# Performance work log

Measured on AMD Instinct MI355X. Metric: run time of the kernel, lower is better.

The kernel has to match this reference:

```python
import jax, jax.numpy as jnp
import numpy as np

B, T, E, H, L = 256, 150, 512, 8, 6
Dh = E // H
FF = 4 * E
NC = 4  # num_decision_classes


def _layer_norm(x, g, b, eps=1e-5):
    m = jnp.mean(x, -1, keepdims=True)
    v = jnp.mean((x - m) ** 2, -1, keepdims=True)
    return (x - m) * jax.lax.rsqrt(v + eps) * g + b


def setup_inputs():
    key = jax.random.key(0)
    ks = jax.random.split(key, 24)
    std = 0.02
    return {
        'token_type': jax.random.randint(ks[0], (B, T), 0, 3, dtype=jnp.int32),
        'mask': jax.random.randint(ks[1], (B, T), 0, 2, dtype=jnp.int32),
        'decision_idx': jax.random.randint(ks[2], (B, T), 0, NC, dtype=jnp.int32),
        'action_val': jax.random.normal(ks[3], (B, T, 1), jnp.float32),
        'dis_val': jax.random.normal(ks[4], (B, T, 10), jnp.float32),
        'v_val': jax.random.normal(ks[5], (B, T, 3), jnp.float32),
        'action_W': jax.random.normal(ks[6], (1, E), jnp.float32) * std,
        'action_b': jnp.zeros((E,), jnp.float32),
        'dis_W': jax.random.normal(ks[7], (10, E), jnp.float32) * std,
        'dis_b': jnp.zeros((E,), jnp.float32),
        'v_W': jax.random.normal(ks[8], (3, E), jnp.float32) * std,
        'v_b': jnp.zeros((E,), jnp.float32),
        'dec_emb': jax.random.normal(ks[9], (NC, E), jnp.float32) * std,
        'pos_embed': jax.random.normal(ks[10], (1, T + 1, E), jnp.float32) * std,
        'cls_token': jax.random.normal(ks[11], (1, 1, E), jnp.float32) * std,
        'qkv_W': jax.random.normal(ks[12], (L, E, 3 * E), jnp.float32) * std,
        'qkv_b': jnp.zeros((L, 3 * E), jnp.float32),
        'out_W': jax.random.normal(ks[13], (L, E, E), jnp.float32) * std,
        'out_b': jnp.zeros((L, E), jnp.float32),
        'ln1_g': jnp.ones((L, E), jnp.float32),
        'ln1_b': jnp.zeros((L, E), jnp.float32),
        'ff1_W': jax.random.normal(ks[14], (L, E, FF), jnp.float32) * std,
        'ff1_b': jnp.zeros((L, FF), jnp.float32),
        'ff2_W': jax.random.normal(ks[15], (L, FF, E), jnp.float32) * std,
        'ff2_b': jnp.zeros((L, E), jnp.float32),
        'ln2_g': jnp.ones((L, E), jnp.float32),
        'ln2_b': jnp.zeros((L, E), jnp.float32),
    }


def reference(token_type, mask, decision_idx, action_val, dis_val, v_val,
              action_W, action_b, dis_W, dis_b, v_W, v_b, dec_emb,
              pos_embed, cls_token, qkv_W, qkv_b, out_W, out_b,
              ln1_g, ln1_b, ff1_W, ff1_b, ff2_W, ff2_b, ln2_g, ln2_b):
    Bx, Tx = token_type.shape
    # vectorized per-type token embedding dispatch (A / S / D)
    a = action_val @ action_W + action_b                       # [B,T,E]
    s = dis_val @ dis_W + dis_b + v_val @ v_W + v_b            # [B,T,E]
    d = dec_emb[decision_idx]                                  # [B,T,E]
    tt = token_type[..., None]
    x = jnp.where(tt == 0, a, jnp.where(tt == 1, s, d))
    x = x + pos_embed[:, :Tx, :]
    x = jnp.concatenate([jnp.broadcast_to(cls_token, (Bx, 1, x.shape[-1])), x], axis=1)
    S = Tx + 1
    pad = jnp.concatenate([jnp.zeros((Bx, 1), bool), mask == 0], axis=1)  # True = padded key
    bias = jnp.where(pad, jnp.float32(-1e9), jnp.float32(0.0))[:, None, None, :]  # [B,1,1,S]
    scale = jnp.float32(1.0 / np.sqrt(Dh))

    def block(x, p):
        qkvW, qkvb, oW, ob, g1, b1, f1W, f1b, f2W, f2b, g2, b2 = p
        qkv = x @ qkvW + qkvb                                  # [B,S,3E]
        q, k, v = jnp.split(qkv, 3, axis=-1)
        hd = lambda t: t.reshape(Bx, S, H, Dh).transpose(0, 2, 1, 3)
        q, k, v = hd(q), hd(k), hd(v)                          # [B,H,S,Dh]
        scores = jnp.einsum('bhqd,bhkd->bhqk', q, k) * scale + bias
        attn = jax.nn.softmax(scores, axis=-1)
        o = jnp.einsum('bhqk,bhkd->bhqd', attn, v).transpose(0, 2, 1, 3).reshape(Bx, S, -1)
        x = _layer_norm(x + o @ oW + ob, g1, b1)               # post-norm (torch default)
        h = jax.nn.relu(x @ f1W + f1b) @ f2W + f2b
        x = _layer_norm(x + h, g2, b2)
        return x, None

    params = (qkv_W, qkv_b, out_W, out_b, ln1_g, ln1_b,
              ff1_W, ff1_b, ff2_W, ff2_b, ln2_g, ln2_b)
    x, _ = jax.lax.scan(block, x, params)
    return x[:, 0, :]  # cls output, mode='pretrain'
```

## Files before the change

### kernel.cpp

```cpp
#include <hip/hip_runtime.h>
#include <hip/hip_bf16.h>
#include <stdint.h>

#define B_ 256
#define T_ 150
#define S_ 151
#define E_ 512
#define H_ 8
#define L_ 6
#define FF_ 2048
#define M_ (B_*S_)

typedef __hip_bfloat16 bf16;
typedef __bf16 bf16x8 __attribute__((ext_vector_type(8)));
typedef float f32x4 __attribute__((ext_vector_type(4)));
typedef unsigned short u16x8 __attribute__((ext_vector_type(8)));

__device__ inline unsigned short f2b(float x) {
    union { __hip_bfloat16 h; unsigned short u; } c;
    c.h = __float2bfloat16(x);
    return c.u;
}
__device__ inline float b2f(unsigned short u) {
    union { uint32_t u; float f; } c;
    c.u = (uint32_t)u << 16;
    return c.f;
}

__device__ __forceinline__ void gl16(const void* g, void* l) {
    __builtin_amdgcn_global_load_lds(
        (const __attribute__((address_space(1))) unsigned int*)g,
        (__attribute__((address_space(3))) unsigned int*)l, 16, 0, 0);
}

__global__ __launch_bounds__(256)
void transpose_cast_kernel(const float* __restrict__ src, bf16* __restrict__ dst,
                           int K, int N) {
    __shared__ float tile[64][65];
    int l = blockIdx.z;
    const float* s = src + (size_t)l * K * N;
    bf16* d = dst + (size_t)l * K * N;
    int bk = blockIdx.x * 64, bn = blockIdx.y * 64;
    int col = threadIdx.x & 63, rg = threadIdx.x >> 6;
#pragma unroll
    for (int i = 0; i < 16; ++i) {
        int r = i * 4 + rg;
        tile[r][col] = s[(size_t)(bk + r) * N + bn + col];
    }
    __syncthreads();
#pragma unroll
    for (int i = 0; i < 16; ++i) {
        int r = i * 4 + rg;
        d[(size_t)(bn + r) * K + bk + col] = __float2bfloat16(tile[col][r]);
    }
}

__global__ __launch_bounds__(256)
void embed_kernel(const int* __restrict__ tt, const int* __restrict__ dec_idx,
                  const float* __restrict__ action_val, const float* __restrict__ dis_val,
                  const float* __restrict__ v_val,
                  const float* __restrict__ action_W, const float* __restrict__ action_b,
                  const float* __restrict__ dis_W, const float* __restrict__ dis_b,
                  const float* __restrict__ v_W, const float* __restrict__ v_b,
                  const float* __restrict__ dec_emb, const float* __restrict__ pos,
                  const float* __restrict__ cls,
                  bf16* __restrict__ xbf) {
    int lane = threadIdx.x & 63;
    int bs = blockIdx.x * 4 + (threadIdx.x >> 6);
    int b = bs / S_, s = bs - b * S_;
    int e0 = lane * 8;
    f32x4 v0, v1;
    if (s == 0) {
        v0 = *(const f32x4*)(cls + e0);
        v1 = *(const f32x4*)(cls + e0 + 4);
    } else {
        int t = s - 1;
        int ty = tt[b * T_ + t];
        if (ty == 0) {
            float av = action_val[b * T_ + t];
            f32x4 w0 = *(const f32x4*)(action_W + e0);
            f32x4 w1 = *(const f32x4*)(action_W + e0 + 4);
            f32x4 b0 = *(const f32x4*)(action_b + e0);
            f32x4 b1 = *(const f32x4*)(action_b + e0 + 4);
            v0 = w0 * av + b0;  v1 = w1 * av + b1;
        } else if (ty == 1) {
            v0 = *(const f32x4*)(dis_b + e0) + *(const f32x4*)(v_b + e0);
            v1 = *(const f32x4*)(dis_b + e0 + 4) + *(const f32x4*)(v_b + e0 + 4);
#pragma unroll
            for (int i = 0; i < 10; ++i) {
                float dv = dis_val[(b * T_ + t) * 10 + i];
                v0 += *(const f32x4*)(dis_W + i * E_ + e0) * dv;
                v1 += *(const f32x4*)(dis_W + i * E_ + e0 + 4) * dv;
            }
#pragma unroll
            for (int i = 0; i < 3; ++i) {
                float vv = v_val[(b * T_ + t) * 3 + i];
                v0 += *(const f32x4*)(v_W + i * E_ + e0) * vv;
                v1 += *(const f32x4*)(v_W + i * E_ + e0 + 4) * vv;
            }
        } else {
            const float* de = dec_emb + (size_t)dec_idx[b * T_ + t] * E_;
            v0 = *(const f32x4*)(de + e0);
            v1 = *(const f32x4*)(de + e0 + 4);
        }
        v0 += *(const f32x4*)(pos + (size_t)t * E_ + e0);
        v1 += *(const f32x4*)(pos + (size_t)t * E_ + e0 + 4);
    }
    size_t o = (size_t)bs * E_ + e0;
    union { unsigned short s[8]; uint4 v; } pk;
    pk.s[0] = f2b(v0[0]); pk.s[1] = f2b(v0[1]); pk.s[2] = f2b(v0[2]); pk.s[3] = f2b(v0[3]);
    pk.s[4] = f2b(v1[0]); pk.s[5] = f2b(v1[1]); pk.s[6] = f2b(v1[2]); pk.s[7] = f2b(v1[3]);
    *(uint4*)((unsigned short*)xbf + o) = pk.v;
}

template<int MODE>
__global__ __launch_bounds__(256, 2)
void gemm_kernel(const bf16* __restrict__ A, const bf16* __restrict__ Bt,
                 const float* __restrict__ bias, bf16* __restrict__ Cb,
                 int N, int K) {
    __shared__ alignas(16) bf16 As[128][64];
    __shared__ alignas(16) bf16 Bs[128][64];
    const int tid = threadIdx.x;
    const int wave = tid >> 6, lane = tid & 63;
    const int nwg = gridDim.x, bid = blockIdx.x;
    const int Nt = N >> 7;
    const int q = nwg >> 3, r = nwg & 7;
    const int xcd = bid & 7, slot = bid >> 3;
    const int wgid = (xcd < r ? xcd * (q + 1) : r * (q + 1) + (xcd - r) * q) + slot;
    const int mt = wgid / Nt, ntl = wgid - mt * Nt;
    const int m0 = mt * 128, n0 = ntl * 128;
    const int wm = (wave >> 1) * 64, wn = (wave & 1) * 64;
    const int l15 = lane & 15, lg = lane >> 4;

    f32x4 acc[4][4] = {};

    for (int k0 = 0; k0 < K; k0 += 64) {
#pragma unroll
        for (int i = 0; i < 4; ++i) {
            int chunk = i * 256 + tid;
            int row = chunk >> 3, cl = chunk & 7;
            int gc = cl ^ (row & 7);
            gl16(A + (size_t)(m0 + row) * K + k0 + gc * 8,
                 (char*)&As[0][0] + chunk * 16);
            gl16(Bt + (size_t)(n0 + row) * K + k0 + gc * 8,
                 (char*)&Bs[0][0] + chunk * 16);
        }
        __syncthreads();
#pragma unroll
        for (int kf = 0; kf < 2; ++kf) {
            bf16x8 af[4], bfr[4];
#pragma unroll
            for (int mf = 0; mf < 4; ++mf) {
                int row = wm + mf * 16 + l15;
                int csw = (kf * 4 + lg) ^ (row & 7);
                af[mf] = *(const bf16x8*)((const char*)&As[0][0] + row * 128 + csw * 16);
            }
#pragma unroll
            for (int nf = 0; nf < 4; ++nf) {
                int row = wn + nf * 16 + l15;
                int csw = (kf * 4 + lg) ^ (row & 7);
                bfr[nf] = *(const bf16x8*)((const char*)&Bs[0][0] + row * 128 + csw * 16);
            }
#pragma unroll
            for (int mf = 0; mf < 4; ++mf)
#pragma unroll
                for (int nf = 0; nf < 4; ++nf)
                    acc[mf][nf] = __builtin_amdgcn_mfma_f32_16x16x32_bf16(
                        af[mf], bfr[nf], acc[mf][nf], 0, 0, 0);
        }
        __syncthreads();
    }
#pragma unroll
    for (int nf = 0; nf < 4; ++nf) {
        int col = n0 + wn + nf * 16 + l15;
        float bv = bias[col];
#pragma unroll
        for (int mf = 0; mf < 4; ++mf) {
#pragma unroll
            for (int j = 0; j < 4; ++j) {
                int row = m0 + wm + mf * 16 + lg * 4 + j;
                size_t idx = (size_t)row * N + col;
                float x = acc[mf][nf][j] + bv;
                if (MODE == 1) x = fmaxf(x, 0.f);
                Cb[idx] = __float2bfloat16(x);
            }
        }
    }
}

#define VP_ 168
__global__ __launch_bounds__(256, 2)
void attn_kernel(const bf16* __restrict__ qkv, const int* __restrict__ mask,
                 bf16* __restrict__ obf) {
    __shared__ alignas(16) unsigned short ldsbuf[32064];
    unsigned short* Kb = ldsbuf;
    unsigned short* QP = ldsbuf + 10240;
    unsigned short* Vt = ldsbuf + 10240 + 10752;
    float* biasf = (float*)(ldsbuf + 10240 + 10752 + 10752);

    const int bh = blockIdx.x;
    const int b = bh >> 3, h = bh & 7;
    const int tid = threadIdx.x, w = tid >> 6, lane = tid & 63;
    const int l15 = lane & 15, lg = lane >> 4;
    const size_t base = (size_t)b * S_ * 1536 + h * 64;
    const unsigned short* qk16 = (const unsigned short*)qkv;

    for (int i = tid; i < 160 * 8; i += 256) {
        int r = i >> 3, c = i & 7;
        int csw = c ^ (r & 7);
        uint4 kz = make_uint4(0u, 0u, 0u, 0u), qz = kz;
        if (r < 151) {
            kz = *(const uint4*)(qk16 + base + (size_t)r * 1536 + 512 + c * 8);
            qz = *(const uint4*)(qk16 + base + (size_t)r * 1536 + c * 8);
        }
        *(uint4*)((char*)Kb + r * 128 + csw * 16) = kz;
        *(uint4*)((char*)QP + r * 128 + csw * 16) = qz;
    }
    for (int i = tid; i < 160 * 8; i += 256) {
        int n = i >> 3, c = i & 7;
        u16x8 vv = {0, 0, 0, 0, 0, 0, 0, 0};
        if (n < 151) vv = *(const u16x8*)(qk16 + base + (size_t)n * 1536 + 1024 + c * 8);
#pragma unroll
        for (int e = 0; e < 8; ++e) Vt[(c * 8 + e) * VP_ + n] = vv[e];
    }
    if (tid < 160) {
        float bv;
        if (tid == 0) bv = 0.f;
        else if (tid <= 150) bv = (mask[b * T_ + tid - 1] != 0) ? 0.f : -1e9f;
        else bv = -1e9f;
        biasf[tid] = bv;
    }
    __syncthreads();

    int r0 = w * 16 + l15;
    int r1 = r0 + 64;
    int r2 = r0 + 128; if (r2 > 159) r2 = 159;
    bf16x8 q00 = *(const bf16x8*)((const char*)QP + r0 * 128 + ((lg)     ^ (r0 & 7)) * 16);
    bf16x8 q01 = *(const bf16x8*)((const char*)QP + r0 * 128 + ((4 + lg) ^ (r0 & 7)) * 16);
    bf16x8 q10 = *(const bf16x8*)((const char*)QP + r1 * 128 + ((lg)     ^ (r1 & 7)) * 16);
    bf16x8 q11 = *(const bf16x8*)((const char*)QP + r1 * 128 + ((4 + lg) ^ (r1 & 7)) * 16);
    bf16x8 q20 = *(const bf16x8*)((const char*)QP + r2 * 128 + ((lg)     ^ (r2 & 7)) * 16);
    bf16x8 q21 = *(const bf16x8*)((const char*)QP + r2 * 128 + ((4 + lg) ^ (r2 & 7)) * 16);
    float bc0 = biasf[l15],       bc1 = biasf[16 + l15],  bc2 = biasf[32 + l15];
    float bc3 = biasf[48 + l15],  bc4 = biasf[64 + l15],  bc5 = biasf[80 + l15];
    float bc6 = biasf[96 + l15],  bc7 = biasf[112 + l15], bc8 = biasf[128 + l15];
    float bc9 = biasf[144 + l15];
    __syncthreads();

    bf16* Pw = (bf16*)(QP + w * 16 * VP_);
    const float scale = 0.125f;

#pragma unroll
    for (int mi = 0; mi < 3; ++mi) {
        int mt = w + mi * 4;
        if (mt < 10) {
            bf16x8 qk0 = (mi == 0) ? q00 : (mi == 1) ? q10 : q20;
            bf16x8 qk1 = (mi == 0) ? q01 : (mi == 1) ? q11 : q21;
            f32x4 sc[10] = {};
#pragma unroll
            for (int nt = 0; nt < 10; ++nt) {
                int kr = nt * 16 + l15;
                bf16x8 kb0 = *(const bf16x8*)((const char*)Kb + kr * 128 + ((lg)     ^ (kr & 7)) * 16);
                bf16x8 kb1 = *(const bf16x8*)((const char*)Kb + kr * 128 + ((4 + lg) ^ (kr & 7)) * 16);
                sc[nt] = __builtin_amdgcn_mfma_f32_16x16x32_bf16(qk0, kb0, sc[nt], 0, 0, 0);
                sc[nt] = __builtin_amdgcn_mfma_f32_16x16x32_bf16(qk1, kb1, sc[nt], 0, 0, 0);
            }
            float m0r = -3e38f, m1r = -3e38f, m2r = -3e38f, m3r = -3e38f;
#pragma unroll
            for (int nt = 0; nt < 10; ++nt) {
                float bv = (nt == 0) ? bc0 : (nt == 1) ? bc1 : (nt == 2) ? bc2 :
                           (nt == 3) ? bc3 : (nt == 4) ? bc4 : (nt == 5) ? bc5 :
                           (nt == 6) ? bc6 : (nt == 7) ? bc7 : (nt == 8) ? bc8 : bc9;
                sc[nt][0] = sc[nt][0] * scale + bv;  m0r = fmaxf(m0r, sc[nt][0]);
                sc[nt][1] = sc[nt][1] * scale + bv;  m1r = fmaxf(m1r, sc[nt][1]);
                sc[nt][2] = sc[nt][2] * scale + bv;  m2r = fmaxf(m2r, sc[nt][2]);
                sc[nt][3] = sc[nt][3] * scale + bv;  m3r = fmaxf(m3r, sc[nt][3]);
            }
#pragma unroll
            for (int off = 1; off < 16; off <<= 1) {
                m0r = fmaxf(m0r, __shfl_xor(m0r, off));
                m1r = fmaxf(m1r, __shfl_xor(m1r, off));
                m2r = fmaxf(m2r, __shfl_xor(m2r, off));
                m3r = fmaxf(m3r, __shfl_xor(m3r, off));
            }
            float s0 = 0.f, s1 = 0.f, s2 = 0.f, s3 = 0.f;
#pragma unroll
            for (int nt = 0; nt < 10; ++nt) {
                sc[nt][0] = __expf(sc[nt][0] - m0r);  s0 += sc[nt][0];
                sc[nt][1] = __expf(sc[nt][1] - m1r);  s1 += sc[nt][1];
                sc[nt][2] = __expf(sc[nt][2] - m2r);  s2 += sc[nt][2];
                sc[nt][3] = __expf(sc[nt][3] - m3r);  s3 += sc[nt][3];
            }
#pragma unroll
            for (int off = 1; off < 16; off <<= 1) {
                s0 += __shfl_xor(s0, off);
                s1 += __shfl_xor(s1, off);
                s2 += __shfl_xor(s2, off);
                s3 += __shfl_xor(s3, off);
            }
            s0 = 1.f / s0; s1 = 1.f / s1; s2 = 1.f / s2; s3 = 1.f / s3;
#pragma unroll
            for (int nt = 0; nt < 10; ++nt) {
                int cb = nt * 16 + l15;
                Pw[(lg * 4 + 0) * VP_ + cb] = __float2bfloat16(sc[nt][0]);
                Pw[(lg * 4 + 1) * VP_ + cb] = __float2bfloat16(sc[nt][1]);
                Pw[(lg * 4 + 2) * VP_ + cb] = __float2bfloat16(sc[nt][2]);
                Pw[(lg * 4 + 3) * VP_ + cb] = __float2bfloat16(sc[nt][3]);
            }
            f32x4 oc[4] = {};
#pragma unroll
            for (int nc = 0; nc < 5; ++nc) {
                bf16x8 pa = *(const bf16x8*)((const unsigned short*)Pw + l15 * VP_ + nc * 32 + lg * 8);
#pragma unroll
                for (int dt = 0; dt < 4; ++dt) {
                    bf16x8 vb = *(const bf16x8*)(Vt + (dt * 16 + l15) * VP_ + nc * 32 + lg * 8);
                    oc[dt] = __builtin_amdgcn_mfma_f32_16x16x32_bf16(pa, vb, oc[dt], 0, 0, 0);
                }
            }
            int orow = mt * 16 + lg * 4;
#pragma unroll
            for (int dt = 0; dt < 4; ++dt) {
                int d = h * 64 + dt * 16 + l15;
                if (orow + 0 < 151) obf[((size_t)(b * S_ + orow + 0)) * E_ + d] = __float2bfloat16(oc[dt][0] * s0);
                if (orow + 1 < 151) obf[((size_t)(b * S_ + orow + 1)) * E_ + d] = __float2bfloat16(oc[dt][1] * s1);
                if (orow + 2 < 151) obf[((size_t)(b * S_ + orow + 2)) * E_ + d] = __float2bfloat16(oc[dt][2] * s2);
                if (orow + 3 < 151) obf[((size_t)(b * S_ + orow + 3)) * E_ + d] = __float2bfloat16(oc[dt][3] * s3);
            }
        }
    }
}

__global__ __launch_bounds__(256)
void ln_res_kernel(const bf16* __restrict__ t_bf, const float* __restrict__ gw,
                   const float* __restrict__ bw, bf16* __restrict__ xbf) {
    int lane = threadIdx.x & 63;
    int row = blockIdx.x * 4 + (threadIdx.x >> 6);
    size_t o = (size_t)row * E_ + lane * 8;
    u16x8 xv = *(const u16x8*)((const unsigned short*)xbf + o);
    u16x8 tv = *(const u16x8*)((const unsigned short*)t_bf + o);
    f32x4 t0, t1;
    t0[0] = b2f(xv[0]) + b2f(tv[0]); t0[1] = b2f(xv[1]) + b2f(tv[1]);
    t0[2] = b2f(xv[2]) + b2f(tv[2]); t0[3] = b2f(xv[3]) + b2f(tv[3]);
    t1[0] = b2f(xv[4]) + b2f(tv[4]); t1[1] = b2f(xv[5]) + b2f(tv[5]);
    t1[2] = b2f(xv[6]) + b2f(tv[6]); t1[3] = b2f(xv[7]) + b2f(tv[7]);
    float s = t0[0] + t0[1] + t0[2] + t0[3] + t1[0] + t1[1] + t1[2] + t1[3];
#pragma unroll
    for (int off = 1; off < 64; off <<= 1) s += __shfl_xor(s, off);
    float mean = s * (1.0f / 512.0f);
    f32x4 d0 = t0 - mean, d1 = t1 - mean;
    float q = d0[0]*d0[0] + d0[1]*d0[1] + d0[2]*d0[2] + d0[3]*d0[3]
            + d1[0]*d1[0] + d1[1]*d1[1] + d1[2]*d1[2] + d1[3]*d1[3];
#pragma unroll
    for (int off = 1; off < 64; off <<= 1) q += __shfl_xor(q, off);
    float rstd = rsqrtf(q * (1.0f / 512.0f) + 1e-5f);
    f32x4 g0 = *(const f32x4*)(gw + lane * 8);
    f32x4 g1 = *(const f32x4*)(gw + lane * 8 + 4);
    f32x4 bb0 = *(const f32x4*)(bw + lane * 8);
    f32x4 bb1 = *(const f32x4*)(bw + lane * 8 + 4);
    f32x4 y0 = d0 * rstd * g0 + bb0;
    f32x4 y1 = d1 * rstd * g1 + bb1;
    union { unsigned short s[8]; uint4 v; } pk;
    pk.s[0] = f2b(y0[0]); pk.s[1] = f2b(y0[1]); pk.s[2] = f2b(y0[2]); pk.s[3] = f2b(y0[3]);
    pk.s[4] = f2b(y1[0]); pk.s[5] = f2b(y1[1]); pk.s[6] = f2b(y1[2]); pk.s[7] = f2b(y1[3]);
    *(uint4*)((unsigned short*)xbf + o) = pk.v;
}

__global__ __launch_bounds__(256)
void out_kernel(const bf16* __restrict__ xbf, float* __restrict__ out) {
    int i = blockIdx.x * 256 + threadIdx.x;
    int b = i >> 9, e = i & 511;
    out[i] = b2f(((const unsigned short*)xbf)[(size_t)b * S_ * E_ + e]);
}

extern "C" void kernel_launch(void* const* d_in, const int* in_sizes, int n_in,
                              void* d_out, int out_size, void* d_ws, size_t ws_size,
                              hipStream_t stream) {
    (void)in_sizes; (void)n_in; (void)out_size; (void)ws_size;
    const int*   token_type = (const int*)d_in[0];
    const int*   mask       = (const int*)d_in[1];
    const int*   dec_idx    = (const int*)d_in[2];
    const float* action_val = (const float*)d_in[3];
    const float* dis_val    = (const float*)d_in[4];
    const float* v_val      = (const float*)d_in[5];
    const float* action_W   = (const float*)d_in[6];
    const float* action_b   = (const float*)d_in[7];
    const float* dis_W      = (const float*)d_in[8];
    const float* dis_b      = (const float*)d_in[9];
    const float* v_W        = (const float*)d_in[10];
    const float* v_b        = (const float*)d_in[11];
    const float* dec_emb    = (const float*)d_in[12];
    const float* pos        = (const float*)d_in[13];
    const float* cls        = (const float*)d_in[14];
    const float* qkv_W      = (const float*)d_in[15];
    const float* qkv_b      = (const float*)d_in[16];
    const float* out_W      = (const float*)d_in[17];
    const float* out_b      = (const float*)d_in[18];
    const float* ln1_g      = (const float*)d_in[19];
    const float* ln1_b      = (const float*)d_in[20];
    const float* ff1_W      = (const float*)d_in[21];
    const float* ff1_b      = (const float*)d_in[22];
    const float* ff2_W      = (const float*)d_in[23];
    const float* ff2_b      = (const float*)d_in[24];
    const float* ln2_g      = (const float*)d_in[25];
    const float* ln2_b      = (const float*)d_in[26];

    char* ws = (char*)d_ws;
    size_t off = 0;
    auto alloc = [&](size_t bytes) {
        char* p = ws + off;
        off += (bytes + 255) & ~(size_t)255;
        return p;
    };
    bf16* qkvT = (bf16*)alloc((size_t)L_ * 1536 * 512 * 2);
    bf16* outT = (bf16*)alloc((size_t)L_ * 512 * 512 * 2);
    bf16* ff1T = (bf16*)alloc((size_t)L_ * 2048 * 512 * 2);
    bf16* ff2T = (bf16*)alloc((size_t)L_ * 512 * 2048 * 2);
    bf16*  xbf = (bf16*)alloc((size_t)M_ * E_ * 2);
    bf16* arena = (bf16*)alloc((size_t)M_ * 2048 * 2);
    bf16* qkvbf  = arena;
    bf16* obf    = arena + (size_t)M_ * 1536;
    bf16* projout= arena;
    bf16* hbf    = arena + (size_t)M_ * 512;
    bf16* t2     = arena + (size_t)M_ * 1536;

    dim3 blk(256);
    transpose_cast_kernel<<<dim3(8, 24, L_), blk, 0, stream>>>(qkv_W, qkvT, 512, 1536);
    transpose_cast_kernel<<<dim3(8, 8,  L_), blk, 0, stream>>>(out_W, outT, 512, 512);
    transpose_cast_kernel<<<dim3(8, 32, L_), blk, 0, stream>>>(ff1_W, ff1T, 512, 2048);
    transpose_cast_kernel<<<dim3(32, 8, L_), blk, 0, stream>>>(ff2_W, ff2T, 2048, 512);

    embed_kernel<<<dim3(M_ / 4), blk, 0, stream>>>(token_type, dec_idx, action_val, dis_val, v_val,
        action_W, action_b, dis_W, dis_b, v_W, v_b, dec_emb, pos, cls, xbf);

    const int HALF_ROWS = 19328;

    for (int l = 0; l < L_; ++l) {
        const bf16* qT = qkvT + (size_t)l * 1536 * 512;
        const bf16* oT = outT + (size_t)l * 512 * 512;
        const bf16* f1 = ff1T + (size_t)l * 2048 * 512;
        const bf16* f2 = ff2T + (size_t)l * 512 * 2048;

        gemm_kernel<3><<<dim3(302 * 12), blk, 0, stream>>>(
            xbf, qT, qkv_b + l * 1536, qkvbf, 1536, 512);
        attn_kernel<<<dim3(B_ * H_), blk, 0, stream>>>(qkvbf, mask, obf);
        gemm_kernel<3><<<dim3(302 * 4), blk, 0, stream>>>(
            obf, oT, out_b + l * 512, projout, 512, 512);
        ln_res_kernel<<<dim3(M_ / 4), blk, 0, stream>>>(
            projout, ln1_g + l * 512, ln1_b + l * 512, xbf);
        for (int c = 0; c < 2; ++c) {
            size_t rb = (size_t)c * HALF_ROWS;
            gemm_kernel<1><<<dim3(151 * 16), blk, 0, stream>>>(
                xbf + rb * E_, f1, ff1_b + l * 2048, hbf, 2048, 512);
            gemm_kernel<3><<<dim3(151 * 4), blk, 0, stream>>>(
                hbf, f2, ff2_b + l * 512, t2, 512, 2048);
            ln_res_kernel<<<dim3(HALF_ROWS / 4), blk, 0, stream>>>(
                t2, ln2_g + l * 512, ln2_b + l * 512, xbf + rb * E_);
        }
    }
    out_kernel<<<dim3(B_ * E_ / 256), blk, 0, stream>>>(xbf, (float*)d_out);
}
```

Baseline: 2.367 ms.

## Add 256x256-tile 8-wave GEMM with ping-pong prefetch for QKV and FF1

```diff
diff --git a/kernel.cpp b/kernel.cpp
--- a/kernel.cpp
+++ b/kernel.cpp
@@ -188,6 +188,144 @@
     }
 }
 
+template<int MODE>
+__global__ __launch_bounds__(512, 1)
+void gemm8p_kernel(const bf16* __restrict__ A, const bf16* __restrict__ Bt,
+                   const float* __restrict__ bias, bf16* __restrict__ Cb,
+                   int Mrows, int N, int K) {
+    extern __shared__ char smem[];
+
+    const int tid = threadIdx.x;
+    const int w = tid >> 6, lane = tid & 63;
+    const int l15 = lane & 15, lg = lane >> 4;
+    const int wr = w >> 2, wc = w & 3;
+
+    const int nwg = gridDim.x, bid = blockIdx.x;
+    const int Ntl = N >> 8;
+    const int q = nwg >> 3, r = nwg & 7;
+    const int xcd = bid & 7, slot = bid >> 3;
+    const int wgid = (xcd < r ? xcd * (q + 1) : r * (q + 1) + (xcd - r) * q) + slot;
+    const int mt = wgid / Ntl, ntl = wgid - mt * Ntl;
+    const int m0 = mt * 256, n0 = ntl * 256;
+
+    const int sw0 = ((lg) ^ (l15 & 7)) * 16;
+    const int sw1 = ((4 + lg) ^ (l15 & 7)) * 16;
+
+    f32x4 acc[8][4] = {};
+
+#define SG_HALF(src, dst, kt, h) do {                                          \
+    _Pragma("unroll")                                                          \
+    for (int i_ = 0; i_ < 2; ++i_) {                                           \
+        int ch_ = (h) * 1024 + i_ * 512 + tid;                                 \
+        int rw_ = ch_ >> 3, cc_ = ch_ & 7;                                     \
+        int gc_ = cc_ ^ (rw_ & 7);                                             \
+        gl16(src + (size_t)rw_ * K + (kt) * 64 + gc_ * 8, dst + ch_ * 16);     \
+    }                                                                          \
+} while (0)
+
+#define LOAD_A(buf, mfB) do {                                                  \
+    _Pragma("unroll")                                                          \
+    for (int ml_ = 0; ml_ < 4; ++ml_) {                                        \
+        int rw_ = wr * 128 + ((mfB) + ml_) * 16 + l15;                         \
+        av[ml_ * 2 + 0] = *(const bf16x8*)((buf) + rw_ * 128 + sw0);           \
+        av[ml_ * 2 + 1] = *(const bf16x8*)((buf) + rw_ * 128 + sw1);           \
+    }                                                                          \
+} while (0)
+
+#define LOAD_B(buf, nfB) do {                                                  \
+    _Pragma("unroll")                                                          \
+    for (int nl_ = 0; nl_ < 2; ++nl_) {                                        \
+        int rw_ = wc * 64 + ((nfB) + nl_) * 16 + l15;                          \
+        bv[nl_ * 2 + 0] = *(const bf16x8*)((buf) + rw_ * 128 + sw0);           \
+        bv[nl_ * 2 + 1] = *(const bf16x8*)((buf) + rw_ * 128 + sw1);           \
+    }                                                                          \
+} while (0)
+
+#define MM(mfB, nfB) do {                                                      \
+    __builtin_amdgcn_s_setprio(1);                                             \
+    _Pragma("unroll")                                                          \
+    for (int ml_ = 0; ml_ < 4; ++ml_) {                                        \
+        _Pragma("unroll")                                                      \
+        for (int nl_ = 0; nl_ < 2; ++nl_) {                                    \
+            _Pragma("unroll")                                                  \
+            for (int kf_ = 0; kf_ < 2; ++kf_) {                                \
+                acc[(mfB) + ml_][(nfB) + nl_] =                                \
+                    __builtin_amdgcn_mfma_f32_16x16x32_bf16(                   \
+                        av[ml_ * 2 + kf_], bv[nl_ * 2 + kf_],                  \
+                        acc[(mfB) + ml_][(nfB) + nl_], 0, 0, 0);               \
+            }                                                                  \
+        }                                                                      \
+    }                                                                          \
+    __builtin_amdgcn_s_setprio(0);                                             \
+} while (0)
+
+    const bf16* Ab = A + (size_t)m0 * K;
+    const bf16* Bb = Bt + (size_t)n0 * K;
+    {
+        char* A0 = smem;
+        char* B0 = smem + 65536;
+        SG_HALF(Ab, A0, 0, 0); SG_HALF(Ab, A0, 0, 1);
+        SG_HALF(Bb, B0, 0, 0); SG_HALF(Bb, B0, 0, 1);
+    }
+
+    const int nt = K >> 6;
+    for (int t = 0; t < nt; ++t) {
+        const int cur = t & 1, nxt = cur ^ 1;
+        const char* cA = smem + cur * 32768;
+        const char* cB = smem + 65536 + cur * 32768;
+        char* nA = smem + nxt * 32768;
+        char* nB = smem + 65536 + nxt * 32768;
+        const bool st = (t + 1 < nt);
+
+        __builtin_amdgcn_sched_barrier(0);
+        asm volatile("s_waitcnt vmcnt(0)" ::: "memory");
+        __builtin_amdgcn_s_barrier();
+        __builtin_amdgcn_sched_barrier(0);
+
+        bf16x8 av[8], bv[4];
+        if (st) SG_HALF(Ab, nA, t + 1, 0);
+        LOAD_A(cA, 0);
+        LOAD_B(cB, 0);
+        MM(0, 0);
+        __builtin_amdgcn_sched_barrier(0);
+        if (st) SG_HALF(Ab, nA, t + 1, 1);
+        LOAD_B(cB, 2);
+        MM(0, 2);
+        __builtin_amdgcn_sched_barrier(0);
+        if (st) SG_HALF(Bb, nB, t + 1, 0);
+        LOAD_A(cA, 4);
+        MM(4, 2);
+        __builtin_amdgcn_sched_barrier(0);
+        if (st) SG_HALF(Bb, nB, t + 1, 1);
+        LOAD_B(cB, 0);
+        MM(4, 0);
+        __builtin_amdgcn_sched_barrier(0);
+    }
+
+#undef SG_HALF
+#undef LOAD_A
+#undef LOAD_B
+#undef MM
+
+#pragma unroll
+    for (int nf = 0; nf < 4; ++nf) {
+        int col = n0 + wc * 64 + nf * 16 + l15;
+        float bvv = bias[col];
+#pragma unroll
+        for (int mf = 0; mf < 8; ++mf) {
+#pragma unroll
+            for (int j = 0; j < 4; ++j) {
+                int row = m0 + wr * 128 + mf * 16 + lg * 4 + j;
+                if (row < Mrows) {
+                    float x = acc[mf][nf][j] + bvv;
+                    if (MODE == 1) x = fmaxf(x, 0.f);
+                    Cb[(size_t)row * N + col] = __float2bfloat16(x);
+                }
+            }
+        }
+    }
+}
+
 #define VP_ 168
 __global__ __launch_bounds__(256, 2)
 void attn_kernel(const bf16* __restrict__ qkv, const int* __restrict__ mask,
@@ -404,6 +542,11 @@
     const float* ln2_g      = (const float*)d_in[25];
     const float* ln2_b      = (const float*)d_in[26];
 
+    (void)hipFuncSetAttribute(reinterpret_cast<const void*>(gemm8p_kernel<3>),
+                        hipFuncAttributeMaxDynamicSharedMemorySize, 131072);
+    (void)hipFuncSetAttribute(reinterpret_cast<const void*>(gemm8p_kernel<1>),
+                        hipFuncAttributeMaxDynamicSharedMemorySize, 131072);
+
     char* ws = (char*)d_ws;
     size_t off = 0;
     auto alloc = [&](size_t bytes) {
@@ -440,8 +583,8 @@
         const bf16* f1 = ff1T + (size_t)l * 2048 * 512;
         const bf16* f2 = ff2T + (size_t)l * 512 * 2048;
 
-        gemm_kernel<3><<<dim3(302 * 12), blk, 0, stream>>>(
-            xbf, qT, qkv_b + l * 1536, qkvbf, 1536, 512);
+        gemm8p_kernel<3><<<dim3(151 * 6), dim3(512), 131072, stream>>>(
+            xbf, qT, qkv_b + l * 1536, qkvbf, M_, 1536, 512);
         attn_kernel<<<dim3(B_ * H_), blk, 0, stream>>>(qkvbf, mask, obf);
         gemm_kernel<3><<<dim3(302 * 4), blk, 0, stream>>>(
             obf, oT, out_b + l * 512, projout, 512, 512);
@@ -449,8 +592,8 @@
             projout, ln1_g + l * 512, ln1_b + l * 512, xbf);
         for (int c = 0; c < 2; ++c) {
             size_t rb = (size_t)c * HALF_ROWS;
-            gemm_kernel<1><<<dim3(151 * 16), blk, 0, stream>>>(
-                xbf + rb * E_, f1, ff1_b + l * 2048, hbf, 2048, 512);
+            gemm8p_kernel<1><<<dim3(76 * 8), dim3(512), 131072, stream>>>(
+                xbf + rb * E_, f1, ff1_b + l * 2048, hbf, HALF_ROWS, 2048, 512);
             gemm_kernel<3><<<dim3(151 * 4), blk, 0, stream>>>(
                 hbf, f2, ff2_b + l * 512, t2, 512, 2048);
             ln_res_kernel<<<dim3(HALF_ROWS / 4), blk, 0, stream>>>(
```

Result: slower. 3.211 ms (+35.7%).

## Compute only CLS row in final layer and merge per-half layernorm launches

Applied to the files above, without the earlier changes.

```diff
diff --git a/kernel.cpp b/kernel.cpp
--- a/kernel.cpp
+++ b/kernel.cpp
@@ -330,6 +330,66 @@
     }
 }
 
+__global__ __launch_bounds__(64)
+void gather_cls_kernel(const bf16* __restrict__ xbf, bf16* __restrict__ xcls) {
+    int b = blockIdx.x, t = threadIdx.x;
+    *(uint4*)((unsigned short*)xcls + (size_t)b * E_ + t * 8) =
+        *(const uint4*)((const unsigned short*)xbf + (size_t)b * S_ * E_ + t * 8);
+}
+
+__global__ __launch_bounds__(256)
+void cls_attn_kernel(const bf16* __restrict__ qcls, const bf16* __restrict__ qkvkv,
+                     const int* __restrict__ mask, bf16* __restrict__ ocls) {
+    __shared__ float q0[64];
+    __shared__ float pb[152];
+    __shared__ float red[8];
+    __shared__ float opart[4][64];
+    const int bh = blockIdx.x, b = bh >> 3, h = bh & 7;
+    const int tid = threadIdx.x, w = tid >> 6, lane = tid & 63;
+    const unsigned short* qk = (const unsigned short*)qkvkv;
+
+    if (tid < 64) q0[tid] = b2f(((const unsigned short*)qcls)[(size_t)b * E_ + h * 64 + tid]);
+    __syncthreads();
+
+    float s = -1e30f;
+    if (tid < 151) {
+        const unsigned short* kr = qk + ((size_t)(b * S_ + tid)) * 1024 + h * 64;
+        float acc = 0.f;
+#pragma unroll
+        for (int c = 0; c < 8; ++c) {
+            u16x8 kv = *(const u16x8*)(kr + c * 8);
+#pragma unroll
+            for (int e = 0; e < 8; ++e) acc += q0[c * 8 + e] * b2f(kv[e]);
+        }
+        float bv = (tid == 0) ? 0.f : ((mask[b * T_ + tid - 1] != 0) ? 0.f : -1e9f);
+        s = acc * 0.125f + bv;
+    }
+    float m = s;
+#pragma unroll
+    for (int off = 1; off < 64; off <<= 1) m = fmaxf(m, __shfl_xor(m, off));
+    if (lane == 0) red[w] = m;
+    __syncthreads();
+    m = fmaxf(fmaxf(red[0], red[1]), fmaxf(red[2], red[3]));
+    float p = (tid < 151) ? __expf(s - m) : 0.f;
+    if (tid < 152) pb[tid] = p;
+    float ss = p;
+#pragma unroll
+    for (int off = 1; off < 64; off <<= 1) ss += __shfl_xor(ss, off);
+    if (lane == 0) red[4 + w] = ss;
+    __syncthreads();
+    float inv = 1.f / (red[4] + red[5] + red[6] + red[7]);
+    int j0 = w * 38, j1 = j0 + 38; if (j1 > 151) j1 = 151;
+    float o = 0.f;
+    for (int j = j0; j < j1; ++j)
+        o += pb[j] * b2f(qk[((size_t)(b * S_ + j)) * 1024 + 512 + h * 64 + lane]);
+    opart[w][lane] = o;
+    __syncthreads();
+    if (tid < 64) {
+        float oo = (opart[0][tid] + opart[1][tid] + opart[2][tid] + opart[3][tid]) * inv;
+        ((unsigned short*)ocls)[(size_t)b * E_ + h * 64 + tid] = f2b(oo);
+    }
+}
+
 __global__ __launch_bounds__(256)
 void ln_res_kernel(const bf16* __restrict__ t_bf, const float* __restrict__ gw,
                    const float* __restrict__ bw, bf16* __restrict__ xbf) {
@@ -366,10 +426,9 @@
 }
 
 __global__ __launch_bounds__(256)
-void out_kernel(const bf16* __restrict__ xbf, float* __restrict__ out) {
+void out_cls_kernel(const bf16* __restrict__ xcls, float* __restrict__ out) {
     int i = blockIdx.x * 256 + threadIdx.x;
-    int b = i >> 9, e = i & 511;
-    out[i] = b2f(((const unsigned short*)xbf)[(size_t)b * S_ * E_ + e]);
+    out[i] = b2f(((const unsigned short*)xcls)[i]);
 }
 
 extern "C" void kernel_launch(void* const* d_in, const int* in_sizes, int n_in,
@@ -422,6 +481,13 @@
     bf16* projout= arena;
     bf16* hbf    = arena + (size_t)M_ * 512;
     bf16* t2     = arena + (size_t)M_ * 1536;
+    bf16* qkvkv = arena;
+    bf16* xcls  = arena + (size_t)M_ * 1024;
+    bf16* qcls  = xcls + 131072;
+    bf16* ocls  = qcls + 131072;
+    bf16* projc = ocls + 131072;
+    bf16* ffh   = projc + 131072;
+    bf16* t2c   = ffh + 524288;
 
     dim3 blk(256);
     transpose_cast_kernel<<<dim3(8, 24, L_), blk, 0, stream>>>(qkv_W, qkvT, 512, 1536);
@@ -434,7 +500,7 @@
 
     const int HALF_ROWS = 19328;
 
-    for (int l = 0; l < L_; ++l) {
+    for (int l = 0; l < 5; ++l) {
         const bf16* qT = qkvT + (size_t)l * 1536 * 512;
         const bf16* oT = outT + (size_t)l * 512 * 512;
         const bf16* f1 = ff1T + (size_t)l * 2048 * 512;
@@ -452,10 +518,35 @@
             gemm_kernel<1><<<dim3(151 * 16), blk, 0, stream>>>(
                 xbf + rb * E_, f1, ff1_b + l * 2048, hbf, 2048, 512);
             gemm_kernel<3><<<dim3(151 * 4), blk, 0, stream>>>(
-                hbf, f2, ff2_b + l * 512, t2, 512, 2048);
-            ln_res_kernel<<<dim3(HALF_ROWS / 4), blk, 0, stream>>>(
-                t2, ln2_g + l * 512, ln2_b + l * 512, xbf + rb * E_);
-        }
-    }
-    out_kernel<<<dim3(B_ * E_ / 256), blk, 0, stream>>>(xbf, (float*)d_out);
-}
+                hbf, f2, ff2_b + l * 512, t2 + rb * E_, 512, 2048);
+        }
+        ln_res_kernel<<<dim3(M_ / 4), blk, 0, stream>>>(
+            t2, ln2_g + l * 512, ln2_b + l * 512, xbf);
+    }
+
+    {
+        const int l = 5;
+        const bf16* qT = qkvT + (size_t)l * 1536 * 512;
+        const bf16* oT = outT + (size_t)l * 512 * 512;
+        const bf16* f1 = ff1T + (size_t)l * 2048 * 512;
+        const bf16* f2 = ff2T + (size_t)l * 512 * 2048;
+
+        gemm_kernel<3><<<dim3(302 * 8), blk, 0, stream>>>(
+            xbf, qT + (size_t)512 * 512, qkv_b + l * 1536 + 512, qkvkv, 1024, 512);
+        gather_cls_kernel<<<dim3(B_), dim3(64), 0, stream>>>(xbf, xcls);
+        gemm_kernel<3><<<dim3(2 * 4), blk, 0, stream>>>(
+            xcls, qT, qkv_b + l * 1536, qcls, 512, 512);
+        cls_attn_kernel<<<dim3(B_ * H_), blk, 0, stream>>>(qcls, qkvkv, mask, ocls);
+        gemm_kernel<3><<<dim3(2 * 4), blk, 0, stream>>>(
+            ocls, oT, out_b + l * 512, projc, 512, 512);
+        ln_res_kernel<<<dim3(B_ / 4), blk, 0, stream>>>(
+            projc, ln1_g + l * 512, ln1_b + l * 512, xcls);
+        gemm_kernel<1><<<dim3(2 * 16), blk, 0, stream>>>(
+            xcls, f1, ff1_b + l * 2048, ffh, 2048, 512);
+        gemm_kernel<3><<<dim3(2 * 4), blk, 0, stream>>>(
+            ffh, f2, ff2_b + l * 512, t2c, 512, 2048);
+        ln_res_kernel<<<dim3(B_ / 4), blk, 0, stream>>>(
+            t2c, ln2_g + l * 512, ln2_b + l * 512, xcls);
+    }
+    out_cls_kernel<<<dim3(B_ * E_ / 256), blk, 0, stream>>>(xcls, (float*)d_out);
+}
```

After: 2.119 ms. -10.5%, faster.
